# Optimization experiments

Measured on AMD Instinct MI355X. Metric: run time of the kernel, lower is better.

The kernel has to match this reference:

```python
import jax, jax.numpy as jnp
import numpy as np

N_NODES = 50000
N_EDGES = 800000
D = 128            # embedding.hidden_size == sage.hidden_channels
SYN_V, LEM_V, POS_V, SEN_V = 120000, 150000, 5, 210000
LN_EPS = 1e-12


def setup_inputs() -> dict:
    key = jax.random.key(0)
    ks = jax.random.split(key, 12)
    s = 0.02
    inp = {
        "x": jax.random.randint(ks[0], (N_NODES, 4), 0, 5, dtype=jnp.int64)
             if jax.config.jax_enable_x64 else jax.random.randint(ks[0], (N_NODES, 4), 0, 5, dtype=jnp.int32),
        "edge_index": jax.random.randint(ks[1], (2, N_EDGES), 0, N_NODES, dtype=jnp.int32),
        "syn_emb": jax.random.normal(ks[2], (SYN_V, D), jnp.float32) * s,
        "lem_emb": jax.random.normal(ks[3], (LEM_V, D), jnp.float32) * s,
        "pos_emb": jax.random.normal(ks[4], (POS_V, D), jnp.float32) * s,
        "sen_emb": jax.random.normal(ks[5], (SEN_V, D), jnp.float32) * s,
        "ln_g": jnp.ones((D,), jnp.float32),
        "ln_b": jnp.zeros((D,), jnp.float32),
        "Wl0": jax.random.normal(ks[6], (D, D), jnp.float32) * s,
        "bl0": jnp.zeros((D,), jnp.float32),
        "Wr0": jax.random.normal(ks[7], (D, D), jnp.float32) * s,
        "Wl1": jax.random.normal(ks[8], (D, D), jnp.float32) * s,
        "bl1": jnp.zeros((D,), jnp.float32),
        "Wr1": jax.random.normal(ks[9], (D, D), jnp.float32) * s,
    }
    return inp


def _layer_norm(h, g, b):
    mu = jnp.mean(h, axis=-1, keepdims=True)
    var = jnp.mean(jnp.square(h - mu), axis=-1, keepdims=True)
    return (h - mu) * jax.lax.rsqrt(var + LN_EPS) * g + b


def _sage_conv(h, src, dst, Wl, bl, Wr, n_nodes):
    # mean-aggregate source neighbor features at each target node
    msg = h[src]                                            # [E, D] gather
    agg = jax.ops.segment_sum(msg, dst, num_segments=n_nodes)
    cnt = jax.ops.segment_sum(jnp.ones((src.shape[0],), h.dtype), dst,
                              num_segments=n_nodes)
    agg = agg / jnp.maximum(cnt, 1.0)[:, None]              # isolated nodes -> 0
    return agg @ Wl.T + bl + h @ Wr.T                       # lin_l(agg)+lin_r(x)


def reference(x, edge_index, syn_emb, lem_emb, pos_emb, sen_emb, ln_g, ln_b,
              Wl0, bl0, Wr0, Wl1, bl1, Wr1):
    # WordnetEmbeddings: sum of 4 lookups, LayerNorm (dropout = eval identity)
    h = (syn_emb[x[:, 0]] + lem_emb[x[:, 3]]
         + pos_emb[x[:, 1]] + sen_emb[x[:, 2]])
    h = _layer_norm(h, ln_g, ln_b)
    src, dst = edge_index[0], edge_index[1]
    n = h.shape[0]
    # SAGE.full_forward, 2 layers, relu between (dropout = eval identity)
    h = _sage_conv(h, src, dst, Wl0, bl0, Wr0, n)
    h = jax.nn.relu(h)
    h = _sage_conv(h, src, dst, Wl1, bl1, Wr1, n)
    return h
```

## Files before the change

### kernel.cpp

```cpp
#include <hip/hip_runtime.h>

#define D 128
#define LN_EPS 1e-12f

typedef unsigned int uint;
typedef unsigned short ushort_t;
typedef __attribute__((ext_vector_type(8))) short bf16x8;
typedef __attribute__((ext_vector_type(4))) float f32x4;

__device__ inline ushort_t f2bf(float f) {
  uint u = __float_as_uint(f);
  u += 0x7fffu + ((u >> 16) & 1u);
  return (ushort_t)(u >> 16);
}
__device__ inline float bf2f(ushort_t h) {
  return __uint_as_float((uint)h << 16);
}
__device__ inline uint pack_bf16(float a, float b) {
  return (uint)f2bf(a) | ((uint)f2bf(b) << 16);
}

__global__ __launch_bounds__(256) void embed_ln_kernel(
    const int* __restrict__ x,
    const float* __restrict__ syn, const float* __restrict__ lem,
    const float* __restrict__ pos, const float* __restrict__ sen,
    const float* __restrict__ g, const float* __restrict__ b,
    ushort_t* __restrict__ hH, ushort_t* __restrict__ hL, int n) {
  int lane = threadIdx.x & 63;
  int q = lane & 31, s = lane >> 5;
  int node = blockIdx.x * 8 + (threadIdx.x >> 6) * 2 + s;
  if (node >= n) return;
  int4 xi = ((const int4*)x)[node];
  float4 v0 = ((const float4*)(syn + (size_t)xi.x * D))[q];
  float4 v1 = ((const float4*)(pos + (size_t)xi.y * D))[q];
  float4 v2 = ((const float4*)(sen + (size_t)xi.z * D))[q];
  float4 v3 = ((const float4*)(lem + (size_t)xi.w * D))[q];
  float4 hs;
  hs.x = v0.x + v1.x + v2.x + v3.x;
  hs.y = v0.y + v1.y + v2.y + v3.y;
  hs.z = v0.z + v1.z + v2.z + v3.z;
  hs.w = v0.w + v1.w + v2.w + v3.w;
  float sum = hs.x + hs.y + hs.z + hs.w;
#pragma unroll
  for (int off = 16; off; off >>= 1) sum += __shfl_xor(sum, off);
  float mu = sum * (1.0f / 128.0f);
  float4 d;
  d.x = hs.x - mu; d.y = hs.y - mu; d.z = hs.z - mu; d.w = hs.w - mu;
  float sq = d.x * d.x + d.y * d.y + d.z * d.z + d.w * d.w;
#pragma unroll
  for (int off = 16; off; off >>= 1) sq += __shfl_xor(sq, off);
  float rstd = rsqrtf(sq * (1.0f / 128.0f) + LN_EPS);
  float4 gg = ((const float4*)g)[q];
  float4 bb = ((const float4*)b)[q];
  float4 o;
  o.x = d.x * rstd * gg.x + bb.x;
  o.y = d.y * rstd * gg.y + bb.y;
  o.z = d.z * rstd * gg.z + bb.z;
  o.w = d.w * rstd * gg.w + bb.w;
  ushort_t hx = f2bf(o.x), hy = f2bf(o.y), hz = f2bf(o.z), hw = f2bf(o.w);
  uint2 ph;
  ph.x = (uint)hx | ((uint)hy << 16);
  ph.y = (uint)hz | ((uint)hw << 16);
  ((uint2*)(hH + (size_t)node * D))[q] = ph;
  uint2 pl;
  pl.x = pack_bf16(o.x - bf2f(hx), o.y - bf2f(hy));
  pl.y = pack_bf16(o.z - bf2f(hz), o.w - bf2f(hw));
  ((uint2*)(hL + (size_t)node * D))[q] = pl;
}

__global__ __launch_bounds__(256) void wprep_kernel(
    const float* __restrict__ Wl0, const float* __restrict__ Wr0,
    const float* __restrict__ Wl1, const float* __restrict__ Wr1,
    ushort_t* __restrict__ Wb0H, ushort_t* __restrict__ Wb0L,
    ushort_t* __restrict__ Wb1H, ushort_t* __restrict__ Wb1L) {
  int idx = blockIdx.x * 256 + threadIdx.x;
  int layer = idx >> 15;
  int e = idx & 32767;
  int col = e >> 8, k = e & 255;
  const float* Wl = layer ? Wl1 : Wl0;
  const float* Wr = layer ? Wr1 : Wr0;
  float v = (k < 128) ? Wl[col * 128 + k] : Wr[col * 128 + (k - 128)];
  ushort_t h = f2bf(v);
  float lo = v - bf2f(h);
  if (layer) {
    Wb1H[e] = h; Wb1L[e] = f2bf(lo);
  } else {
    Wb0H[e] = h; Wb0L[e] = f2bf(lo);
  }
}

__global__ __launch_bounds__(256) void hist_kernel(const int* __restrict__ dst,
                                                   int* __restrict__ counts,
                                                   int nEdges) {
  int e = blockIdx.x * 256 + threadIdx.x;
  if (e < nEdges) atomicAdd(&counts[dst[e]], 1);
}

__global__ __launch_bounds__(256) void scan_part_kernel(
    const int* __restrict__ counts, int* __restrict__ partials) {
  int t = threadIdx.x;
  int base = blockIdx.x * 1024 + t * 4;
  int4 v = *(const int4*)(counts + base);
  int s = v.x + v.y + v.z + v.w;
#pragma unroll
  for (int off = 1; off < 64; off <<= 1) s += __shfl_xor(s, off);
  __shared__ int ws[4];
  if ((t & 63) == 0) ws[t >> 6] = s;
  __syncthreads();
  if (t == 0) partials[blockIdx.x] = ws[0] + ws[1] + ws[2] + ws[3];
}

__global__ __launch_bounds__(256) void scan_write_kernel(
    const int* __restrict__ counts, const int* __restrict__ partials,
    int* __restrict__ row_ptr, int n, int E) {
  int t = threadIdx.x;
  int b = blockIdx.x;
  int off = 0;
  for (int i = 0; i < b; ++i) off += partials[i];
  int base = b * 1024 + t * 4;
  int4 v = *(const int4*)(counts + base);
  int s = v.x + v.y + v.z + v.w;
  int lane = t & 63;
  int incl = s;
#pragma unroll
  for (int dd = 1; dd < 64; dd <<= 1) {
    int u = __shfl_up(incl, dd);
    if (lane >= dd) incl += u;
  }
  __shared__ int wsum[4];
  if (lane == 63) wsum[t >> 6] = incl;
  __syncthreads();
  int wid = t >> 6;
  int wpre = 0;
#pragma unroll
  for (int w = 0; w < 4; ++w)
    if (w < wid) wpre += wsum[w];
  int excl = off + wpre + incl - s;
  int4 r;
  r.x = excl;
  r.y = excl + v.x;
  r.z = r.y + v.y;
  r.w = r.z + v.z;
  if (base + 3 < n) {
    *(int4*)(row_ptr + base) = r;
  } else {
    if (base < n) row_ptr[base] = r.x;
    if (base + 1 < n) row_ptr[base + 1] = r.y;
    if (base + 2 < n) row_ptr[base + 2] = r.z;
    if (base + 3 < n) row_ptr[base + 3] = r.w;
  }
  if (b == 0 && t == 0) row_ptr[n] = E;
}

__global__ __launch_bounds__(256) void fill_kernel(const int* __restrict__ src,
                                                   const int* __restrict__ dst,
                                                   const int* __restrict__ row_ptr,
                                                   int* __restrict__ cursor,
                                                   int* __restrict__ adj,
                                                   int nEdges) {
  int e = blockIdx.x * 256 + threadIdx.x;
  if (e >= nEdges) return;
  int d = dst[e];
  int p = atomicAdd(&cursor[d], 1);
  adj[row_ptr[d] + p] = src[e];
}

__global__ __launch_bounds__(256) void gather_bf16_kernel(
    const int* __restrict__ row_ptr, const int* __restrict__ adj,
    const ushort_t* __restrict__ hb,
    ushort_t* __restrict__ aggH, ushort_t* __restrict__ aggL, int n) {
  int node = blockIdx.x * 4 + (threadIdx.x >> 6);
  if (node >= n) return;
  int lane = threadIdx.x & 63;
  int q = lane & 15, s = lane >> 4;
  int beg = row_ptr[node], end = row_ptr[node + 1];
  int count = end - beg;
  float a0 = 0.f, a1 = 0.f, a2 = 0.f, a3 = 0.f;
  float a4 = 0.f, a5 = 0.f, a6 = 0.f, a7 = 0.f;
  int lim = beg + (count & ~7);
  for (int bb = beg; bb < lim; bb += 8) {
    int e0 = adj[bb + s], e1 = adj[bb + 4 + s];
    uint4 v0 = ((const uint4*)(hb + (size_t)e0 * D))[q];
    uint4 v1 = ((const uint4*)(hb + (size_t)e1 * D))[q];
    a0 += __uint_as_float(v0.x << 16) + __uint_as_float(v1.x << 16);
    a1 += __uint_as_float(v0.x & 0xffff0000u) + __uint_as_float(v1.x & 0xffff0000u);
    a2 += __uint_as_float(v0.y << 16) + __uint_as_float(v1.y << 16);
    a3 += __uint_as_float(v0.y & 0xffff0000u) + __uint_as_float(v1.y & 0xffff0000u);
    a4 += __uint_as_float(v0.z << 16) + __uint_as_float(v1.z << 16);
    a5 += __uint_as_float(v0.z & 0xffff0000u) + __uint_as_float(v1.z & 0xffff0000u);
    a6 += __uint_as_float(v0.w << 16) + __uint_as_float(v1.w << 16);
    a7 += __uint_as_float(v0.w & 0xffff0000u) + __uint_as_float(v1.w & 0xffff0000u);
  }
  for (int i = lim + s; i < end; i += 4) {
    int e0 = adj[i];
    uint4 v0 = ((const uint4*)(hb + (size_t)e0 * D))[q];
    a0 += __uint_as_float(v0.x << 16);
    a1 += __uint_as_float(v0.x & 0xffff0000u);
    a2 += __uint_as_float(v0.y << 16);
    a3 += __uint_as_float(v0.y & 0xffff0000u);
    a4 += __uint_as_float(v0.z << 16);
    a5 += __uint_as_float(v0.z & 0xffff0000u);
    a6 += __uint_as_float(v0.w << 16);
    a7 += __uint_as_float(v0.w & 0xffff0000u);
  }
#pragma unroll
  for (int off = 16; off <= 32; off <<= 1) {
    a0 += __shfl_xor(a0, off); a1 += __shfl_xor(a1, off);
    a2 += __shfl_xor(a2, off); a3 += __shfl_xor(a3, off);
    a4 += __shfl_xor(a4, off); a5 += __shfl_xor(a5, off);
    a6 += __shfl_xor(a6, off); a7 += __shfl_xor(a7, off);
  }
  if (s == 0) {
    float inv = 1.0f / fmaxf((float)count, 1.0f);
    float v0 = a0 * inv, v1 = a1 * inv, v2 = a2 * inv, v3 = a3 * inv;
    float v4 = a4 * inv, v5 = a5 * inv, v6 = a6 * inv, v7 = a7 * inv;
    ushort_t h0 = f2bf(v0), h1 = f2bf(v1), h2 = f2bf(v2), h3 = f2bf(v3);
    ushort_t h4 = f2bf(v4), h5 = f2bf(v5), h6 = f2bf(v6), h7 = f2bf(v7);
    uint4 ph;
    ph.x = (uint)h0 | ((uint)h1 << 16);
    ph.y = (uint)h2 | ((uint)h3 << 16);
    ph.z = (uint)h4 | ((uint)h5 << 16);
    ph.w = (uint)h6 | ((uint)h7 << 16);
    uint4 pl;
    pl.x = pack_bf16(v0 - bf2f(h0), v1 - bf2f(h1));
    pl.y = pack_bf16(v2 - bf2f(h2), v3 - bf2f(h3));
    pl.z = pack_bf16(v4 - bf2f(h4), v5 - bf2f(h5));
    pl.w = pack_bf16(v6 - bf2f(h6), v7 - bf2f(h7));
    *(uint4*)(aggH + (size_t)node * D + q * 8) = ph;
    *(uint4*)(aggL + (size_t)node * D + q * 8) = pl;
  }
}

__global__ __launch_bounds__(256) void sage_mfma_kernel(
    const ushort_t* __restrict__ aggH, const ushort_t* __restrict__ aggL,
    const ushort_t* hinH, const ushort_t* hinL,
    const ushort_t* __restrict__ WbH, const ushort_t* __restrict__ WbL,
    const float* __restrict__ bias,
    float* outF, ushort_t* outH, ushort_t* outL, int n, int doRelu) {
  __shared__ ushort_t AsH[64 * 64];
  __shared__ ushort_t AsL[64 * 64];
  __shared__ ushort_t BsH[128 * 64];
  __shared__ ushort_t BsL[128 * 64];
  int tid = threadIdx.x;
  int lane = tid & 63;
  int wave = tid >> 6;
  int base = blockIdx.x * 64;
  int wr = (wave & 1) * 32;
  int wc = (wave >> 1) * 64;

  f32x4 zero = {0.f, 0.f, 0.f, 0.f};
  f32x4 acc[2][4];
#pragma unroll
  for (int i = 0; i < 2; ++i)
#pragma unroll
    for (int j = 0; j < 4; ++j) acc[i][j] = zero;

  int arow = tid >> 2;
  int anode = base + arow;
  if (anode >= n) anode = n - 1;
  int akb = (tid & 3) * 32;
  int aswz = (arow & 7) << 4;
  char* aHdst = (char*)AsH + arow * 128;
  char* aLdst = (char*)AsL + arow * 128;

  int bcol = tid >> 1;
  int bkb = (tid & 1) * 64;
  int bswz = (bcol & 7) << 4;
  char* bHdst = (char*)BsH + bcol * 128;
  char* bLdst = (char*)BsL + bcol * 128;
  const ushort_t* wHsrc = WbH + (size_t)bcol * 256 + (tid & 1) * 32;
  const ushort_t* wLsrc = WbL + (size_t)bcol * 256 + (tid & 1) * 32;

  for (int kc = 0; kc < 4; ++kc) {
    {
      const ushort_t* sH = (kc < 2 ? aggH : hinH) +
                           (size_t)anode * D + (kc & 1) * 64 + (tid & 3) * 16;
      const ushort_t* sL = (kc < 2 ? aggL : hinL) +
                           (size_t)anode * D + (kc & 1) * 64 + (tid & 3) * 16;
      uint4 h0 = *(const uint4*)sH;
      uint4 h1 = *(const uint4*)(sH + 8);
      uint4 l0 = *(const uint4*)sL;
      uint4 l1 = *(const uint4*)(sL + 8);
      *(uint4*)(aHdst + ((akb) ^ aswz)) = h0;
      *(uint4*)(aHdst + ((akb + 16) ^ aswz)) = h1;
      *(uint4*)(aLdst + ((akb) ^ aswz)) = l0;
      *(uint4*)(aLdst + ((akb + 16) ^ aswz)) = l1;
    }
    {
      const ushort_t* sH = wHsrc + kc * 64;
      const ushort_t* sL = wLsrc + kc * 64;
      uint4 h0 = *(const uint4*)sH;
      uint4 h1 = *(const uint4*)(sH + 8);
      uint4 h2 = *(const uint4*)(sH + 16);
      uint4 h3 = *(const uint4*)(sH + 24);
      uint4 l0 = *(const uint4*)sL;
      uint4 l1 = *(const uint4*)(sL + 8);
      uint4 l2 = *(const uint4*)(sL + 16);
      uint4 l3 = *(const uint4*)(sL + 24);
      *(uint4*)(bHdst + ((bkb) ^ bswz)) = h0;
      *(uint4*)(bHdst + ((bkb + 16) ^ bswz)) = h1;
      *(uint4*)(bHdst + ((bkb + 32) ^ bswz)) = h2;
      *(uint4*)(bHdst + ((bkb + 48) ^ bswz)) = h3;
      *(uint4*)(bLdst + ((bkb) ^ bswz)) = l0;
      *(uint4*)(bLdst + ((bkb + 16) ^ bswz)) = l1;
      *(uint4*)(bLdst + ((bkb + 32) ^ bswz)) = l2;
      *(uint4*)(bLdst + ((bkb + 48) ^ bswz)) = l3;
    }
    __syncthreads();
#pragma unroll
    for (int ks = 0; ks < 2; ++ks) {
      int kb = ks * 64 + (lane >> 4) * 16;
      bf16x8 aHf[2], aLf[2], bHf[4], bLf[4];
#pragma unroll
      for (int rf = 0; rf < 2; ++rf) {
        int r = wr + rf * 16 + (lane & 15);
        int off = r * 128 + (kb ^ ((r & 7) << 4));
        aHf[rf] = *(const bf16x8*)((const char*)AsH + off);
        aLf[rf] = *(const bf16x8*)((const char*)AsL + off);
      }
#pragma unroll
      for (int cf = 0; cf < 4; ++cf) {
        int c = wc + cf * 16 + (lane & 15);
        int off = c * 128 + (kb ^ ((c & 7) << 4));
        bHf[cf] = *(const bf16x8*)((const char*)BsH + off);
        bLf[cf] = *(const bf16x8*)((const char*)BsL + off);
      }
#pragma unroll
      for (int rf = 0; rf < 2; ++rf)
#pragma unroll
        for (int cf = 0; cf < 4; ++cf) {
          acc[rf][cf] = __builtin_amdgcn_mfma_f32_16x16x32_bf16(
              aHf[rf], bHf[cf], acc[rf][cf], 0, 0, 0);
          acc[rf][cf] = __builtin_amdgcn_mfma_f32_16x16x32_bf16(
              aHf[rf], bLf[cf], acc[rf][cf], 0, 0, 0);
          acc[rf][cf] = __builtin_amdgcn_mfma_f32_16x16x32_bf16(
              aLf[rf], bHf[cf], acc[rf][cf], 0, 0, 0);
        }
    }
    __syncthreads();
  }

#pragma unroll
  for (int cf = 0; cf < 4; ++cf) {
    int j = wc + cf * 16 + (lane & 15);
    float bj = bias[j];
#pragma unroll
    for (int rf = 0; rf < 2; ++rf) {
      int r0 = base + wr + rf * 16 + (lane >> 4) * 4;
#pragma unroll
      for (int reg = 0; reg < 4; ++reg) {
        int node = r0 + reg;
        if (node >= n) continue;
        float v = acc[rf][cf][reg] + bj;
        if (doRelu) v = fmaxf(v, 0.f);
        if (outF) outF[(size_t)node * D + j] = v;
        if (outH) {
          ushort_t h = f2bf(v);
          outH[(size_t)node * D + j] = h;
          outL[(size_t)node * D + j] = f2bf(v - bf2f(h));
        }
      }
    }
  }
}

extern "C" void kernel_launch(void* const* d_in, const int* in_sizes, int n_in,
                              void* d_out, int out_size, void* d_ws,
                              size_t ws_size, hipStream_t stream) {
  const int* x = (const int*)d_in[0];
  const int* edge = (const int*)d_in[1];
  const float* syn = (const float*)d_in[2];
  const float* lem = (const float*)d_in[3];
  const float* pos = (const float*)d_in[4];
  const float* sen = (const float*)d_in[5];
  const float* ln_g = (const float*)d_in[6];
  const float* ln_b = (const float*)d_in[7];
  const float* Wl0 = (const float*)d_in[8];
  const float* bl0 = (const float*)d_in[9];
  const float* Wr0 = (const float*)d_in[10];
  const float* Wl1 = (const float*)d_in[11];
  const float* bl1 = (const float*)d_in[12];
  const float* Wr1 = (const float*)d_in[13];

  int n = in_sizes[0] / 4;
  int E = in_sizes[1] / 2;
  const int* srcI = edge;
  const int* dstI = edge + E;
  float* outp = (float*)d_out;

  size_t rowElems = (size_t)n * D;
  int nPad = (n + 1023) & ~1023;
  int scanBlocks = nPad >> 10;
  int rpElems = (n + 4) & ~3;
  ushort_t* h0H = (ushort_t*)d_ws;
  ushort_t* h0L = h0H + rowElems;
  ushort_t* aggH = h0L + rowElems;
  ushort_t* aggL = aggH + rowElems;
  ushort_t* Wb0H = aggL + rowElems;
  ushort_t* Wb0L = Wb0H + 32768;
  ushort_t* Wb1H = Wb0L + 32768;
  ushort_t* Wb1L = Wb1H + 32768;
  int* row_ptr = (int*)(Wb1L + 32768);
  int* counts = row_ptr + rpElems;
  int* cursor = counts + nPad;
  int* partials = cursor + n;
  int* adj = partials + scanBlocks;

  hipMemsetAsync(counts, 0, ((size_t)nPad + n) * sizeof(int), stream);

  embed_ln_kernel<<<(n + 7) / 8, 256, 0, stream>>>(x, syn, lem, pos, sen, ln_g,
                                                   ln_b, h0H, h0L, n);

  int eBlocks = (E + 255) / 256;
  hist_kernel<<<eBlocks, 256, 0, stream>>>(dstI, counts, E);
  scan_part_kernel<<<scanBlocks, 256, 0, stream>>>(counts, partials);
  scan_write_kernel<<<scanBlocks, 256, 0, stream>>>(counts, partials, row_ptr,
                                                    n, E);
  fill_kernel<<<eBlocks, 256, 0, stream>>>(srcI, dstI, row_ptr, cursor, adj, E);

  wprep_kernel<<<256, 256, 0, stream>>>(Wl0, Wr0, Wl1, Wr1, Wb0H, Wb0L, Wb1H,
                                        Wb1L);

  int gBlocks = (n + 3) / 4;
  int sBlocks = (n + 63) / 64;

  gather_bf16_kernel<<<gBlocks, 256, 0, stream>>>(row_ptr, adj, h0H, aggH,
                                                  aggL, n);
  sage_mfma_kernel<<<sBlocks, 256, 0, stream>>>(aggH, aggL, h0H, h0L, Wb0H,
                                                Wb0L, bl0, nullptr, h0H, h0L,
                                                n, 1);
  gather_bf16_kernel<<<gBlocks, 256, 0, stream>>>(row_ptr, adj, h0H, aggH,
                                                  aggL, n);
  sage_mfma_kernel<<<sBlocks, 256, 0, stream>>>(aggH, aggL, h0H, h0L, Wb1H,
                                                Wb1L, bl1, outp, nullptr,
                                                nullptr, n, 0);
}
```

Measured before the change: 435.9 us.

## Merge embed, histogram and weight-prep into one launch; enlarge SAGE GEMM row tile

The embedding+LayerNorm, edge-degree histogram and weight bf16 split kernels now run as block ranges of a single front kernel, removing two launches and letting the independent work overlap. The SAGE MFMA kernel now processes 128 rows per block instead of 64, with each wave holding a 4x4 accumulator grid, so each staged weight tile serves twice as many rows. This raises LDS use to 64KB and increases register pressure, which can lower occupancy, and halves the number of GEMM blocks.

```diff
diff --git a/kernel.cpp b/kernel.cpp
--- a/kernel.cpp
+++ b/kernel.cpp
@@ -20,15 +20,44 @@
   return (uint)f2bf(a) | ((uint)f2bf(b) << 16);
 }
 
-__global__ __launch_bounds__(256) void embed_ln_kernel(
+__global__ __launch_bounds__(256) void front_kernel(
     const int* __restrict__ x,
     const float* __restrict__ syn, const float* __restrict__ lem,
     const float* __restrict__ pos, const float* __restrict__ sen,
     const float* __restrict__ g, const float* __restrict__ b,
-    ushort_t* __restrict__ hH, ushort_t* __restrict__ hL, int n) {
+    ushort_t* __restrict__ hH, ushort_t* __restrict__ hL, int n,
+    const int* __restrict__ dst, int* __restrict__ counts, int nEdges,
+    const float* __restrict__ Wl0, const float* __restrict__ Wr0,
+    const float* __restrict__ Wl1, const float* __restrict__ Wr1,
+    ushort_t* __restrict__ Wb0H, ushort_t* __restrict__ Wb0L,
+    ushort_t* __restrict__ Wb1H, ushort_t* __restrict__ Wb1L,
+    int embB, int histB) {
+  int blk = blockIdx.x;
+  if (blk >= embB + histB) {
+    int idx = (blk - embB - histB) * 256 + threadIdx.x;
+    int layer = idx >> 15;
+    int e = idx & 32767;
+    int col = e >> 8, k = e & 255;
+    const float* Wl = layer ? Wl1 : Wl0;
+    const float* Wr = layer ? Wr1 : Wr0;
+    float v = (k < 128) ? Wl[col * 128 + k] : Wr[col * 128 + (k - 128)];
+    ushort_t h = f2bf(v);
+    float lo = v - bf2f(h);
+    if (layer) {
+      Wb1H[e] = h; Wb1L[e] = f2bf(lo);
+    } else {
+      Wb0H[e] = h; Wb0L[e] = f2bf(lo);
+    }
+    return;
+  }
+  if (blk >= embB) {
+    int e = (blk - embB) * 256 + threadIdx.x;
+    if (e < nEdges) atomicAdd(&counts[dst[e]], 1);
+    return;
+  }
   int lane = threadIdx.x & 63;
   int q = lane & 31, s = lane >> 5;
-  int node = blockIdx.x * 8 + (threadIdx.x >> 6) * 2 + s;
+  int node = blk * 8 + (threadIdx.x >> 6) * 2 + s;
   if (node >= n) return;
   int4 xi = ((const int4*)x)[node];
   float4 v0 = ((const float4*)(syn + (size_t)xi.x * D))[q];
@@ -66,34 +95,6 @@
   pl.x = pack_bf16(o.x - bf2f(hx), o.y - bf2f(hy));
   pl.y = pack_bf16(o.z - bf2f(hz), o.w - bf2f(hw));
   ((uint2*)(hL + (size_t)node * D))[q] = pl;
-}
-
-__global__ __launch_bounds__(256) void wprep_kernel(
-    const float* __restrict__ Wl0, const float* __restrict__ Wr0,
-    const float* __restrict__ Wl1, const float* __restrict__ Wr1,
-    ushort_t* __restrict__ Wb0H, ushort_t* __restrict__ Wb0L,
-    ushort_t* __restrict__ Wb1H, ushort_t* __restrict__ Wb1L) {
-  int idx = blockIdx.x * 256 + threadIdx.x;
-  int layer = idx >> 15;
-  int e = idx & 32767;
-  int col = e >> 8, k = e & 255;
-  const float* Wl = layer ? Wl1 : Wl0;
-  const float* Wr = layer ? Wr1 : Wr0;
-  float v = (k < 128) ? Wl[col * 128 + k] : Wr[col * 128 + (k - 128)];
-  ushort_t h = f2bf(v);
-  float lo = v - bf2f(h);
-  if (layer) {
-    Wb1H[e] = h; Wb1L[e] = f2bf(lo);
-  } else {
-    Wb0H[e] = h; Wb0L[e] = f2bf(lo);
-  }
-}
-
-__global__ __launch_bounds__(256) void hist_kernel(const int* __restrict__ dst,
-                                                   int* __restrict__ counts,
-                                                   int nEdges) {
-  int e = blockIdx.x * 256 + threadIdx.x;
-  if (e < nEdges) atomicAdd(&counts[dst[e]], 1);
 }
 
 __global__ __launch_bounds__(256) void scan_part_kernel(
@@ -237,54 +238,59 @@
     const ushort_t* __restrict__ WbH, const ushort_t* __restrict__ WbL,
     const float* __restrict__ bias,
     float* outF, ushort_t* outH, ushort_t* outL, int n, int doRelu) {
-  __shared__ ushort_t AsH[64 * 64];
-  __shared__ ushort_t AsL[64 * 64];
+  __shared__ ushort_t AsH[128 * 64];
+  __shared__ ushort_t AsL[128 * 64];
   __shared__ ushort_t BsH[128 * 64];
   __shared__ ushort_t BsL[128 * 64];
   int tid = threadIdx.x;
   int lane = tid & 63;
   int wave = tid >> 6;
-  int base = blockIdx.x * 64;
-  int wr = (wave & 1) * 32;
+  int base = blockIdx.x * 128;
+  int wr = (wave & 1) * 64;
   int wc = (wave >> 1) * 64;
 
   f32x4 zero = {0.f, 0.f, 0.f, 0.f};
-  f32x4 acc[2][4];
-#pragma unroll
-  for (int i = 0; i < 2; ++i)
+  f32x4 acc[4][4];
+#pragma unroll
+  for (int i = 0; i < 4; ++i)
 #pragma unroll
     for (int j = 0; j < 4; ++j) acc[i][j] = zero;
 
-  int arow = tid >> 2;
-  int anode = base + arow;
+  int row = tid >> 1;
+  int half = tid & 1;
+  int kb0 = half * 64;
+  int swz = (row & 7) << 4;
+  char* aHdst = (char*)AsH + row * 128;
+  char* aLdst = (char*)AsL + row * 128;
+  char* bHdst = (char*)BsH + row * 128;
+  char* bLdst = (char*)BsL + row * 128;
+  int anode = base + row;
   if (anode >= n) anode = n - 1;
-  int akb = (tid & 3) * 32;
-  int aswz = (arow & 7) << 4;
-  char* aHdst = (char*)AsH + arow * 128;
-  char* aLdst = (char*)AsL + arow * 128;
-
-  int bcol = tid >> 1;
-  int bkb = (tid & 1) * 64;
-  int bswz = (bcol & 7) << 4;
-  char* bHdst = (char*)BsH + bcol * 128;
-  char* bLdst = (char*)BsL + bcol * 128;
-  const ushort_t* wHsrc = WbH + (size_t)bcol * 256 + (tid & 1) * 32;
-  const ushort_t* wLsrc = WbL + (size_t)bcol * 256 + (tid & 1) * 32;
+  const ushort_t* wHsrc = WbH + (size_t)row * 256 + half * 32;
+  const ushort_t* wLsrc = WbL + (size_t)row * 256 + half * 32;
 
   for (int kc = 0; kc < 4; ++kc) {
     {
       const ushort_t* sH = (kc < 2 ? aggH : hinH) +
-                           (size_t)anode * D + (kc & 1) * 64 + (tid & 3) * 16;
+                           (size_t)anode * D + (kc & 1) * 64 + half * 32;
       const ushort_t* sL = (kc < 2 ? aggL : hinL) +
-                           (size_t)anode * D + (kc & 1) * 64 + (tid & 3) * 16;
+                           (size_t)anode * D + (kc & 1) * 64 + half * 32;
       uint4 h0 = *(const uint4*)sH;
       uint4 h1 = *(const uint4*)(sH + 8);
+      uint4 h2 = *(const uint4*)(sH + 16);
+      uint4 h3 = *(const uint4*)(sH + 24);
       uint4 l0 = *(const uint4*)sL;
       uint4 l1 = *(const uint4*)(sL + 8);
-      *(uint4*)(aHdst + ((akb) ^ aswz)) = h0;
-      *(uint4*)(aHdst + ((akb + 16) ^ aswz)) = h1;
-      *(uint4*)(aLdst + ((akb) ^ aswz)) = l0;
-      *(uint4*)(aLdst + ((akb + 16) ^ aswz)) = l1;
+      uint4 l2 = *(const uint4*)(sL + 16);
+      uint4 l3 = *(const uint4*)(sL + 24);
+      *(uint4*)(aHdst + ((kb0) ^ swz)) = h0;
+      *(uint4*)(aHdst + ((kb0 + 16) ^ swz)) = h1;
+      *(uint4*)(aHdst + ((kb0 + 32) ^ swz)) = h2;
+      *(uint4*)(aHdst + ((kb0 + 48) ^ swz)) = h3;
+      *(uint4*)(aLdst + ((kb0) ^ swz)) = l0;
+      *(uint4*)(aLdst + ((kb0 + 16) ^ swz)) = l1;
+      *(uint4*)(aLdst + ((kb0 + 32) ^ swz)) = l2;
+      *(uint4*)(aLdst + ((kb0 + 48) ^ swz)) = l3;
     }
     {
       const ushort_t* sH = wHsrc + kc * 64;
@@ -297,22 +303,22 @@
       uint4 l1 = *(const uint4*)(sL + 8);
       uint4 l2 = *(const uint4*)(sL + 16);
       uint4 l3 = *(const uint4*)(sL + 24);
-      *(uint4*)(bHdst + ((bkb) ^ bswz)) = h0;
-      *(uint4*)(bHdst + ((bkb + 16) ^ bswz)) = h1;
-      *(uint4*)(bHdst + ((bkb + 32) ^ bswz)) = h2;
-      *(uint4*)(bHdst + ((bkb + 48) ^ bswz)) = h3;
-      *(uint4*)(bLdst + ((bkb) ^ bswz)) = l0;
-      *(uint4*)(bLdst + ((bkb + 16) ^ bswz)) = l1;
-      *(uint4*)(bLdst + ((bkb + 32) ^ bswz)) = l2;
-      *(uint4*)(bLdst + ((bkb + 48) ^ bswz)) = l3;
+      *(uint4*)(bHdst + ((kb0) ^ swz)) = h0;
+      *(uint4*)(bHdst + ((kb0 + 16) ^ swz)) = h1;
+      *(uint4*)(bHdst + ((kb0 + 32) ^ swz)) = h2;
+      *(uint4*)(bHdst + ((kb0 + 48) ^ swz)) = h3;
+      *(uint4*)(bLdst + ((kb0) ^ swz)) = l0;
+      *(uint4*)(bLdst + ((kb0 + 16) ^ swz)) = l1;
+      *(uint4*)(bLdst + ((kb0 + 32) ^ swz)) = l2;
+      *(uint4*)(bLdst + ((kb0 + 48) ^ swz)) = l3;
     }
     __syncthreads();
 #pragma unroll
     for (int ks = 0; ks < 2; ++ks) {
       int kb = ks * 64 + (lane >> 4) * 16;
-      bf16x8 aHf[2], aLf[2], bHf[4], bLf[4];
-#pragma unroll
-      for (int rf = 0; rf < 2; ++rf) {
+      bf16x8 aHf[4], aLf[4], bHf[4], bLf[4];
+#pragma unroll
+      for (int rf = 0; rf < 4; ++rf) {
         int r = wr + rf * 16 + (lane & 15);
         int off = r * 128 + (kb ^ ((r & 7) << 4));
         aHf[rf] = *(const bf16x8*)((const char*)AsH + off);
@@ -326,7 +332,7 @@
         bLf[cf] = *(const bf16x8*)((const char*)BsL + off);
       }
 #pragma unroll
-      for (int rf = 0; rf < 2; ++rf)
+      for (int rf = 0; rf < 4; ++rf)
 #pragma unroll
         for (int cf = 0; cf < 4; ++cf) {
           acc[rf][cf] = __builtin_amdgcn_mfma_f32_16x16x32_bf16(
@@ -345,7 +351,7 @@
     int j = wc + cf * 16 + (lane & 15);
     float bj = bias[j];
 #pragma unroll
-    for (int rf = 0; rf < 2; ++rf) {
+    for (int rf = 0; rf < 4; ++rf) {
       int r0 = base + wr + rf * 16 + (lane >> 4) * 4;
 #pragma unroll
       for (int reg = 0; reg < 4; ++reg) {
@@ -408,21 +414,21 @@
 
   hipMemsetAsync(counts, 0, ((size_t)nPad + n) * sizeof(int), stream);
 
-  embed_ln_kernel<<<(n + 7) / 8, 256, 0, stream>>>(x, syn, lem, pos, sen, ln_g,
-                                                   ln_b, h0H, h0L, n);
-
-  int eBlocks = (E + 255) / 256;
-  hist_kernel<<<eBlocks, 256, 0, stream>>>(dstI, counts, E);
+  int embB = (n + 7) / 8;
+  int histB = (E + 255) / 256;
+  front_kernel<<<embB + histB + 256, 256, 0, stream>>>(
+      x, syn, lem, pos, sen, ln_g, ln_b, h0H, h0L, n,
+      dstI, counts, E,
+      Wl0, Wr0, Wl1, Wr1, Wb0H, Wb0L, Wb1H, Wb1L,
+      embB, histB);
+
   scan_part_kernel<<<scanBlocks, 256, 0, stream>>>(counts, partials);
   scan_write_kernel<<<scanBlocks, 256, 0, stream>>>(counts, partials, row_ptr,
                                                     n, E);
-  fill_kernel<<<eBlocks, 256, 0, stream>>>(srcI, dstI, row_ptr, cursor, adj, E);
-
-  wprep_kernel<<<256, 256, 0, stream>>>(Wl0, Wr0, Wl1, Wr1, Wb0H, Wb0L, Wb1H,
-                                        Wb1L);
+  fill_kernel<<<histB, 256, 0, stream>>>(srcI, dstI, row_ptr, cursor, adj, E);
 
   int gBlocks = (n + 3) / 4;
-  int sBlocks = (n + 63) / 64;
+  int sBlocks = (n + 127) / 128;
 
   gather_bf16_kernel<<<gBlocks, 256, 0, stream>>>(row_ptr, adj, h0H, aggH,
                                                   aggL, n);
```

Measured after the change: 423.7 us. 2.8% less time.
